# Kernel optimization log

Hardware: AMD Instinct MI355X
Metric: run time of the kernel (lower is better)

The kernel has to match this reference:

```python
import jax, jax.numpy as jnp
import numpy as np

PS = 8          # patch size
D_STATE = 16
D_CONV = 4
DT_RANK = 6     # ceil(96/16)
N_HEADS = 2
NEG = jnp.float32(-1e30)
_DIRS = np.array([[-1, 0], [1, 0], [0, -1], [0, 1]], np.int32)


def _ln(x, w, b, eps=1e-5):
    mu = x.mean(-1, keepdims=True)
    var = ((x - mu) ** 2).mean(-1, keepdims=True)
    return (x - mu) * jax.lax.rsqrt(var + eps) * w + b


def _vit_score_map(x, pos_embed, proj_w, proj_b, in_w, in_b, out_w, out_b,
                   ln1_w, ln1_b, ff1_w, ff1_b, ff2_w, ff2_b, ln2_w, ln2_b,
                   score_w, score_b):
    B, C, H, W = x.shape
    Hp, Wp = H // PS, W // PS
    N = Hp * Wp
    E = proj_w.shape[0]
    # F.unfold ordering: per patch the vector is (C, kr, kc) flattened
    patches = x.reshape(B, C, Hp, PS, Wp, PS).transpose(0, 2, 4, 1, 3, 5).reshape(B, N, C * PS * PS)
    patches = patches @ proj_w.T + proj_b
    if pos_embed.shape[1] != N:
        o = int(pos_embed.shape[1] ** 0.5)
        pe = jax.image.resize(pos_embed.reshape(1, o, o, E), (1, Hp, Wp, E), 'bilinear').reshape(1, N, E)
    else:
        pe = pos_embed
    patches = patches + 0.1 * pe
    # nn.TransformerEncoderLayer defaults: post-norm, ReLU, eval (no dropout)
    qkv = patches @ in_w.T + in_b
    q, k, v = jnp.split(qkv, 3, axis=-1)
    dh = E // N_HEADS
    def heads(t):
        return t.reshape(B, N, N_HEADS, dh).transpose(0, 2, 1, 3)
    q, k, v = heads(q), heads(k), heads(v)
    attn = jax.nn.softmax(jnp.einsum('bhqd,bhkd->bhqk', q, k) / np.float32(np.sqrt(dh)), axis=-1)
    ctx = jnp.einsum('bhqk,bhkd->bhqd', attn, v).transpose(0, 2, 1, 3).reshape(B, N, E)
    src = _ln(patches + (ctx @ out_w.T + out_b), ln1_w, ln1_b)
    ff = jax.nn.relu(src @ ff1_w.T + ff1_b) @ ff2_w.T + ff2_b
    src = _ln(src + ff, ln2_w, ln2_b)
    scores = jax.nn.sigmoid((src @ score_w.T + score_b)[..., 0])
    pvar = patches.var(axis=-1, ddof=1)          # torch.var is unbiased
    final = 0.7 * scores + 0.3 * jax.nn.sigmoid(pvar * 10.0)
    return final.reshape(B, Hp, Wp)


def _traversal(score):
    """Greedy adaptive patch traversal: start at global argmax, walk to the best
    unvisited 4-neighbor; on dead-end jump to the global argmax over unvisited."""
    Hp, Wp = score.shape
    n = Hp * Wp
    s = score.reshape(-1)
    dirs = jnp.asarray(_DIRS)
    start = jnp.argmax(s).astype(jnp.int32)
    visited0 = jnp.zeros((n,), bool).at[start].set(True)

    def step(carry, _):
        visited, cur = carry
        ci, cj = cur // Wp, cur % Wp
        ni, nj = ci + dirs[:, 0], cj + dirs[:, 1]
        valid = (ni >= 0) & (ni < Hp) & (nj >= 0) & (nj < Wp)
        nidx = (jnp.clip(ni, 0, Hp - 1) * Wp + jnp.clip(nj, 0, Wp - 1)).astype(jnp.int32)
        nsc = jnp.where(valid & ~visited[nidx], s[nidx], NEG)
        b = jnp.argmax(nsc)                       # first-max tie-break == '>' loop order
        jump = jnp.argmax(jnp.where(visited, NEG, s)).astype(jnp.int32)
        nxt = jnp.where(nsc[b] > NEG * 0.5, nidx[b], jump).astype(jnp.int32)
        return (visited.at[nxt].set(True), nxt), nxt

    _, rest = jax.lax.scan(step, (visited0, start), None, length=n - 1)
    return jnp.concatenate([start[None], rest])


def _mamba(u, in_w, conv_w, conv_b, xproj_w, dt_w, dt_b, A_log, D_skip, out_w):
    B, L, _ = u.shape
    d_in = conv_w.shape[0]
    xz = u @ in_w.T                               # (B,L,2*d_in)
    xx, z = jnp.split(xz, 2, axis=-1)
    # causal depthwise conv over sequence
    xc = jnp.pad(xx.transpose(0, 2, 1), ((0, 0), (0, 0), (D_CONV - 1, 0)))
    xc = jax.lax.conv_general_dilated(xc, conv_w, (1,), 'VALID',
                                      feature_group_count=d_in,
                                      dimension_numbers=('NCH', 'OIH', 'NCH'))
    xx = jax.nn.silu((xc + conv_b[None, :, None]).transpose(0, 2, 1))   # (B,L,d_in)
    dbl = xx @ xproj_w.T
    dt, Bm, Cm = jnp.split(dbl, [DT_RANK, DT_RANK + D_STATE], axis=-1)
    dt = jax.nn.softplus(dt @ dt_w.T + dt_b)      # (B,L,d_in)
    A = -jnp.exp(A_log)                           # (d_in, d_state)

    def step(h, inp):
        dt_t, B_t, C_t, x_t = inp                 # (B,d_in),(B,ds),(B,ds),(B,d_in)
        h = jnp.exp(dt_t[..., None] * A) * h + (dt_t * x_t)[..., None] * B_t[:, None, :]
        return h, jnp.einsum('bds,bs->bd', h, C_t)

    h0 = jnp.zeros((B, d_in, D_STATE), u.dtype)
    xs = (dt.transpose(1, 0, 2), Bm.transpose(1, 0, 2), Cm.transpose(1, 0, 2), xx.transpose(1, 0, 2))
    _, ys = jax.lax.scan(step, h0, xs)
    y = ys.transpose(1, 0, 2) + xx * D_skip
    return (y * jax.nn.silu(z)) @ out_w.T


def setup_inputs() -> dict:
    key = jax.random.key(0)
    ks = jax.random.split(key, 20)
    B, C, H, W = 2, 96, 128, 128
    E, FF = 96, 2048
    d_in, dr, ds, dc = 192, 6, 16, 4
    f32 = jnp.float32
    def w(k, shape, s=0.02):
        return jax.random.normal(k, shape, f32) * s
    return dict(
        x=jax.random.normal(ks[0], (B, C, H, W), f32),
        pe=w(ks[1], (B, H * W, C), 0.02),
        pos_embed=w(ks[2], (1, 784, E)),
        vit_proj_w=w(ks[3], (E, C * PS * PS)),
        vit_proj_b=jnp.zeros((E,), f32),
        attn_in_w=w(ks[4], (3 * E, E)),
        attn_in_b=jnp.zeros((3 * E,), f32),
        attn_out_w=w(ks[5], (E, E)),
        attn_out_b=jnp.zeros((E,), f32),
        ln1_w=jnp.ones((E,), f32), ln1_b=jnp.zeros((E,), f32),
        ff1_w=w(ks[6], (FF, E)), ff1_b=jnp.zeros((FF,), f32),
        ff2_w=w(ks[7], (E, FF)), ff2_b=jnp.zeros((E,), f32),
        ln2_w=jnp.ones((E,), f32), ln2_b=jnp.zeros((E,), f32),
        score_w=w(ks[8], (1, E)), score_b=jnp.zeros((1,), f32),
        norm_w=jnp.ones((C,), f32), norm_b=jnp.zeros((C,), f32),
        in_proj_w=w(ks[9], (2 * d_in, C)),
        conv_w=w(ks[10], (d_in, 1, dc), 0.1),
        conv_b=jnp.zeros((d_in,), f32),
        x_proj_w=w(ks[11], (dr + 2 * ds, d_in)),
        dt_w=w(ks[12], (d_in, dr)),
        dt_b=jnp.full((d_in,), -4.6, f32),        # softplus(dt_b) ~ 0.01 (mamba dt init)
        A_log=jnp.log(jnp.tile(jnp.arange(1, ds + 1, dtype=f32), (d_in, 1))),
        D_skip=jnp.ones((d_in,), f32),
        out_proj_w=w(ks[13], (C, d_in)),
    )


def reference(x, pe, pos_embed, vit_proj_w, vit_proj_b, attn_in_w, attn_in_b,
              attn_out_w, attn_out_b, ln1_w, ln1_b, ff1_w, ff1_b, ff2_w, ff2_b,
              ln2_w, ln2_b, score_w, score_b, norm_w, norm_b, in_proj_w,
              conv_w, conv_b, x_proj_w, dt_w, dt_b, A_log, D_skip, out_proj_w):
    B, C, H, W = x.shape
    n = H * W
    # Dynamic_Adaptive_Scan with the code's DCNv3Function-is-None fallback:
    # x = input_last, permuted back to channels-first => identity on x.
    x_adapted = x
    score_map = _vit_score_map(x_adapted, pos_embed, vit_proj_w, vit_proj_b,
                               attn_in_w, attn_in_b, attn_out_w, attn_out_b,
                               ln1_w, ln1_b, ff1_w, ff1_b, ff2_w, ff2_b,
                               ln2_w, ln2_b, score_w, score_b)
    order = jax.vmap(_traversal)(jax.lax.stop_gradient(score_map))    # (B, Hp*Wp)
    Hp, Wp = score_map.shape[1], score_map.shape[2]
    pi, pj = order // Wp, order % Wp
    # expand each patch into its PSxPS pixels in raster order
    offs = (jnp.arange(PS, dtype=jnp.int32)[:, None] * W + jnp.arange(PS, dtype=jnp.int32)[None, :]).reshape(-1)
    idx = ((pi * PS * W + pj * PS)[..., None] + offs).reshape(B, n)    # (B, n)
    x_tok = jnp.take_along_axis(x_adapted.reshape(B, C, n), idx[:, None, :], axis=2).transpose(0, 2, 1)
    pe_r = jnp.take_along_axis(pe, idx[..., None], axis=1)
    tokens = _ln(x_tok + pe_r, norm_w, norm_b)
    y = _mamba(tokens, in_proj_w, conv_w, conv_b, x_proj_w, dt_w, dt_b, A_log, D_skip, out_proj_w)
    # scatter back to spatial raster order
    out = jax.vmap(lambda yb, ib: jnp.zeros_like(yb).at[ib].set(yb))(y, idx)
    return out.transpose(0, 2, 1).reshape(B, C, H, W)
```

## Files before the change

kernel.cpp:

```cpp
#include <hip/hip_runtime.h>
#include <math.h>

#define BB 2
#define CC 96
#define HH 128
#define WW 128
#define PS 8
#define HP 16
#define WP 16
#define NPATCH 256
#define EE 96
#define FF 2048
#define DH 48
#define DIN 192
#define DR 6
#define DS 16
#define LL 16384
#define NCHUNK 512
#define CLEN 32
#define NSEG 16
#define SEGC 32
#define KTOT 6144
#define KSPLIT 32
#define KSL 192

__device__ __forceinline__ float sigmoid_acc(float x){ return 1.f/(1.f+expf(-x)); }
__device__ __forceinline__ float sigmoid_fast(float x){ return 1.f/(1.f+__expf(-x)); }

__global__ void k_resize_pe(const float* __restrict__ pos, float* __restrict__ pe16){
  int n = blockIdx.x;
  int oi = n / WP, oj = n % WP;
  int e = threadIdx.x;
  const float inv = 1.75f;
  float sfi = (oi + 0.5f)*inv - 0.5f;
  float sfj = (oj + 0.5f)*inv - 0.5f;
  int i0 = max(0, (int)ceilf(sfi - inv)), i1 = min(27, (int)floorf(sfi + inv));
  int j0 = max(0, (int)ceilf(sfj - inv)), j1 = min(27, (int)floorf(sfj + inv));
  float si = 0.f, sj = 0.f;
  for(int j=i0;j<=i1;j++) si += fmaxf(0.f, 1.f - fabsf(sfi - (float)j)/inv);
  for(int j=j0;j<=j1;j++) sj += fmaxf(0.f, 1.f - fabsf(sfj - (float)j)/inv);
  float acc = 0.f;
  for(int ji=i0;ji<=i1;ji++){
    float wv = fmaxf(0.f, 1.f - fabsf(sfi - (float)ji)/inv) / si;
    for(int jj=j0;jj<=j1;jj++){
      float wu = fmaxf(0.f, 1.f - fabsf(sfj - (float)jj)/inv);
      acc += wv * (wu/sj) * pos[(ji*28+jj)*EE + e];
    }
  }
  pe16[n*EE + e] = acc;
}

__global__ void k_wtr(const float* __restrict__ vw, float* __restrict__ Wt){
  __shared__ float t[64*97];
  int k0 = blockIdx.x*64;
  int tid = threadIdx.x;
  for(int i=tid;i<64*EE;i+=256){
    int e = i>>6, kk = i&63;
    t[kk*97 + e] = vw[(size_t)e*KTOT + k0 + kk];
  }
  __syncthreads();
  for(int i=tid;i<64*EE;i+=256){
    int kk = i/EE, e = i%EE;
    Wt[(size_t)(k0+kk)*EE + e] = t[kk*97 + e];
  }
}

__global__ __launch_bounds__(384) void k_pproj(const float* __restrict__ x,
    const float* __restrict__ Wt, float* __restrict__ part){
  __shared__ float As[16*196];
  int bidx = blockIdx.x;
  int ks = bidx & (KSPLIT-1);
  int pb = bidx >> 5;
  int b = pb >> 4, pi = pb & 15;
  int c0 = ks*3;
  int tid = threadIdx.x;
  for(int i=tid;i<24*128;i+=384){
    int row = i>>7;
    int col = i&127;
    int cl = row>>3, dr = row&7;
    float v = x[(((size_t)(b*CC + c0+cl))<<14) + (size_t)((pi*PS+dr)<<7) + col];
    As[(col>>3)*196 + cl*64 + dr*8 + (col&7)] = v;
  }
  __syncthreads();
  int e = tid % EE;
  int pq = tid / EE;
  const float* wp = Wt + (size_t)(ks*KSL)*EE + e;
  float acc0=0.f, acc1=0.f, acc2=0.f, acc3=0.f;
  const float4* A0 = (const float4*)(As + (pq*4+0)*196);
  const float4* A1 = (const float4*)(As + (pq*4+1)*196);
  const float4* A2 = (const float4*)(As + (pq*4+2)*196);
  const float4* A3 = (const float4*)(As + (pq*4+3)*196);
  #pragma unroll 4
  for(int k4=0;k4<48;k4++){
    float w0 = wp[(k4*4+0)*EE];
    float w1 = wp[(k4*4+1)*EE];
    float w2 = wp[(k4*4+2)*EE];
    float w3 = wp[(k4*4+3)*EE];
    float4 a;
    a = A0[k4]; acc0 += a.x*w0 + a.y*w1 + a.z*w2 + a.w*w3;
    a = A1[k4]; acc1 += a.x*w0 + a.y*w1 + a.z*w2 + a.w*w3;
    a = A2[k4]; acc2 += a.x*w0 + a.y*w1 + a.z*w2 + a.w*w3;
    a = A3[k4]; acc3 += a.x*w0 + a.y*w1 + a.z*w2 + a.w*w3;
  }
  size_t gp0 = (size_t)b*NPATCH + pi*WP + pq*4;
  part[((size_t)ks*512 + gp0+0)*EE + e] = acc0;
  part[((size_t)ks*512 + gp0+1)*EE + e] = acc1;
  part[((size_t)ks*512 + gp0+2)*EE + e] = acc2;
  part[((size_t)ks*512 + gp0+3)*EE + e] = acc3;
}

__global__ __launch_bounds__(320) void k_preduce_qkv(const float* __restrict__ part,
    const float* __restrict__ pb, const float* __restrict__ pe16,
    const float* __restrict__ inw, const float* __restrict__ inb,
    float* __restrict__ patches, float* __restrict__ pvar, float* __restrict__ qkv){
  int gp = blockIdx.x;
  int n = gp % NPATCH;
  int tid = threadIdx.x;
  __shared__ float a[EE];
  __shared__ float ps[2], pq2[2];
  float v = 0.f;
  if(tid < EE){
    float s = 0.f;
    #pragma unroll 8
    for(int ks=0;ks<KSPLIT;ks++) s += part[((size_t)ks*512 + gp)*EE + tid];
    v = s + pb[tid] + 0.1f*pe16[n*EE + tid];
    a[tid] = v;
    patches[(size_t)gp*EE + tid] = v;
  }
  if(tid < 128){
    float sv = v, sq = v*v;
    for(int off=32; off>0; off>>=1){ sv += __shfl_xor(sv, off); sq += __shfl_xor(sq, off); }
    if((tid&63)==0){ ps[tid>>6]=sv; pq2[tid>>6]=sq; }
  }
  __syncthreads();
  if(tid==0){
    float s = ps[0]+ps[1], qq = pq2[0]+pq2[1];
    float mu = s/EE;
    pvar[gp] = (qq - EE*mu*mu)/(EE-1);
  }
  if(tid < 288){
    const float4* ar = (const float4*)a;
    const float4* wr = (const float4*)(inw + (size_t)tid*EE);
    float4 s4 = {0.f,0.f,0.f,0.f};
    #pragma unroll
    for(int k=0;k<24;k++){
      float4 av=ar[k], wv=wr[k];
      s4.x += av.x*wv.x; s4.y += av.y*wv.y; s4.z += av.z*wv.z; s4.w += av.w*wv.w;
    }
    qkv[(size_t)gp*288 + tid] = inb[tid] + (s4.x+s4.y)+(s4.z+s4.w);
  }
}

__global__ void k_attn(const float* __restrict__ qkv, float* __restrict__ ctx){
  int gb = blockIdx.x;
  int i = gb % NPATCH; int h = (gb/NPATCH)&1; int b = gb/(NPATCH*2);
  int tid = threadIdx.x;
  __shared__ float q[DH];
  __shared__ float p[NPATCH];
  __shared__ float red[NPATCH];
  __shared__ float red2[4][DH];
  const float* base = qkv + (size_t)b*NPATCH*288;
  if(tid < DH) q[tid] = base[(size_t)i*288 + h*DH + tid];
  __syncthreads();
  float sc;
  {
    const float4* krow = (const float4*)(base + (size_t)tid*288 + 96 + h*DH);
    const float4* q4 = (const float4*)q;
    float4 s4 = {0.f,0.f,0.f,0.f};
    #pragma unroll
    for(int k=0;k<12;k++){
      float4 kv=krow[k], qv=q4[k];
      s4.x += qv.x*kv.x; s4.y += qv.y*kv.y; s4.z += qv.z*kv.z; s4.w += qv.w*kv.w;
    }
    sc = ((s4.x+s4.y)+(s4.z+s4.w)) * 0.14433756729740643f;
  }
  red[tid] = sc; __syncthreads();
  for(int st=128; st>0; st>>=1){ if(tid<st) red[tid]=fmaxf(red[tid],red[tid+st]); __syncthreads(); }
  float mx = red[0]; __syncthreads();
  float ev = expf(sc - mx);
  red[tid] = ev; __syncthreads();
  for(int st=128; st>0; st>>=1){ if(tid<st) red[tid]+=red[tid+st]; __syncthreads(); }
  float denom = red[0]; __syncthreads();
  p[tid] = ev/denom;
  __syncthreads();
  if(tid < 192){
    int jg = tid/DH, dd = tid%DH;
    const float* vb = base + 192 + h*DH + dd;
    float acc0 = 0.f, acc1 = 0.f;
    #pragma unroll 4
    for(int j=jg*64; j<jg*64+64; j+=2){
      acc0 += p[j]*vb[(size_t)j*288];
      acc1 += p[j+1]*vb[(size_t)(j+1)*288];
    }
    red2[jg][dd] = acc0+acc1;
  }
  __syncthreads();
  if(tid < DH){
    ctx[((size_t)b*NPATCH + i)*EE + h*DH + tid] =
      red2[0][tid]+red2[1][tid]+red2[2][tid]+red2[3][tid];
  }
}

__global__ void k_ln1(const float* __restrict__ ctx, const float* __restrict__ ow,
                      const float* __restrict__ ob, const float* __restrict__ patches,
                      const float* __restrict__ lw, const float* __restrict__ lb,
                      float* __restrict__ src1){
  int row = blockIdx.x; int tid = threadIdx.x;
  __shared__ float a[EE];
  __shared__ float ps[2], pq2[2], st[2];
  if(tid < EE) a[tid] = ctx[(size_t)row*EE + tid];
  __syncthreads();
  float o = 0.f;
  if(tid < EE){
    const float4* ar = (const float4*)a;
    const float4* wr = (const float4*)(ow + (size_t)tid*EE);
    float4 s4 = {0.f,0.f,0.f,0.f};
    #pragma unroll
    for(int k=0;k<24;k++){
      float4 av=ar[k], wv=wr[k];
      s4.x += av.x*wv.x; s4.y += av.y*wv.y; s4.z += av.z*wv.z; s4.w += av.w*wv.w;
    }
    o = ob[tid] + (s4.x+s4.y)+(s4.z+s4.w) + patches[(size_t)row*EE + tid];
  }
  float sv = o, sq = o*o;
  for(int off=32; off>0; off>>=1){ sv += __shfl_xor(sv, off); sq += __shfl_xor(sq, off); }
  if((tid&63)==0){ ps[tid>>6]=sv; pq2[tid>>6]=sq; }
  __syncthreads();
  if(tid==0){
    float s = ps[0]+ps[1], qq = pq2[0]+pq2[1];
    float mu = s/EE;
    st[0]=mu; st[1]=rsqrtf(qq/EE - mu*mu + 1e-5f);
  }
  __syncthreads();
  if(tid < EE) src1[(size_t)row*EE + tid] = (o-st[0])*st[1]*lw[tid] + lb[tid];
}

__global__ __launch_bounds__(512) void k_ff1(const float* __restrict__ src1,
    const float* __restrict__ w1, const float* __restrict__ b1, float* __restrict__ ffh){
  int row0 = blockIdx.x*2; int tid = threadIdx.x;
  const float4* a0 = (const float4*)(src1 + (size_t)row0*EE);
  const float4* a1 = (const float4*)(src1 + (size_t)(row0+1)*EE);
  for(int fo=0;fo<4;fo++){
    int f = fo*512 + tid;
    const float4* wr = (const float4*)(w1 + (size_t)f*EE);
    float bc = b1[f];
    float acc0=bc, acc1=bc;
    #pragma unroll
    for(int k=0;k<24;k++){
      float4 wv = wr[k];
      float4 av;
      av = a0[k]; acc0 += av.x*wv.x+av.y*wv.y+av.z*wv.z+av.w*wv.w;
      av = a1[k]; acc1 += av.x*wv.x+av.y*wv.y+av.z*wv.z+av.w*wv.w;
    }
    ffh[(size_t)(row0+0)*FF + f] = fmaxf(acc0, 0.f);
    ffh[(size_t)(row0+1)*FF + f] = fmaxf(acc1, 0.f);
  }
}

__global__ __launch_bounds__(384) void k_ff2(const float* __restrict__ ffh,
    const float* __restrict__ w2, const float* __restrict__ b2,
    const float* __restrict__ src1, float* __restrict__ src2){
  __shared__ float partl[8][EE];
  int row0 = blockIdx.x*2; int tid = threadIdx.x;
  int e = tid % EE, fg = tid / EE;
  const float4* wr = (const float4*)(w2 + (size_t)e*FF + fg*512);
  const float4* h0 = (const float4*)(ffh + (size_t)row0*FF + fg*512);
  const float4* h1 = (const float4*)(ffh + (size_t)(row0+1)*FF + fg*512);
  float acc0=0.f, acc1=0.f;
  #pragma unroll 4
  for(int k=0;k<128;k++){
    float4 wv = wr[k];
    float4 hv;
    hv = h0[k]; acc0 += hv.x*wv.x+hv.y*wv.y+hv.z*wv.z+hv.w*wv.w;
    hv = h1[k]; acc1 += hv.x*wv.x+hv.y*wv.y+hv.z*wv.z+hv.w*wv.w;
  }
  partl[0*4+fg][e] = acc0;
  partl[1*4+fg][e] = acc1;
  __syncthreads();
  if(tid < 192){
    int r = tid / EE, e2 = tid % EE;
    float s = partl[r*4+0][e2] + partl[r*4+1][e2] + partl[r*4+2][e2] + partl[r*4+3][e2];
    src2[(size_t)(row0+r)*EE + e2] = s + b2[e2] + src1[(size_t)(row0+r)*EE + e2];
  }
}

__global__ void k_ln2_score(const float* __restrict__ src2,
    const float* __restrict__ lw, const float* __restrict__ lb,
    const float* __restrict__ sw, const float* __restrict__ sb,
    const float* __restrict__ pvar, float* __restrict__ fscore){
  int row = blockIdx.x; int tid = threadIdx.x;
  float v = (tid < EE) ? src2[(size_t)row*EE + tid] : 0.f;
  float sv = v, sq = v*v;
  for(int off=32; off>0; off>>=1){ sv += __shfl_xor(sv, off); sq += __shfl_xor(sq, off); }
  __shared__ float ps[2], pq2[2], st[2];
  int wid = tid>>6;
  if((tid&63)==0){ ps[wid]=sv; pq2[wid]=sq; }
  __syncthreads();
  if(tid==0){
    float s = ps[0]+ps[1], qq = pq2[0]+pq2[1];
    float mu = s/EE;
    st[0]=mu; st[1]=rsqrtf(qq/EE - mu*mu + 1e-5f);
  }
  __syncthreads();
  float o = (tid < EE) ? ((v-st[0])*st[1]*lw[tid] + lb[tid]) * sw[tid] : 0.f;
  for(int off=32; off>0; off>>=1) o += __shfl_xor(o, off);
  if((tid&63)==0) ps[wid] = o;
  __syncthreads();
  if(tid==0){
    float acc = ps[0]+ps[1] + sb[0];
    fscore[row] = 0.7f*sigmoid_acc(acc) + 0.3f*sigmoid_acc(pvar[row]*10.f);
  }
}

__global__ void k_traversal(const float* __restrict__ fscore, int* __restrict__ order){
  int b = blockIdx.x; int lane = threadIdx.x;
  __shared__ float fsl[NPATCH];
  __shared__ int   sidxl[NPATCH];
  for(int k=lane;k<NPATCH;k+=64) fsl[k] = fscore[b*NPATCH+k];
  __syncthreads();
  {
    float s0=fsl[lane], s1=fsl[64+lane], s2=fsl[128+lane], s3=fsl[192+lane];
    int i0=lane, i1=64+lane, i2=128+lane, i3=192+lane;
    int c0=0,c1=0,c2=0,c3=0;
    for(int j=0;j<NPATCH;j++){
      float sj=fsl[j];
      c0 += (sj>s0 || (sj==s0 && j<i0)) ? 1:0;
      c1 += (sj>s1 || (sj==s1 && j<i1)) ? 1:0;
      c2 += (sj>s2 || (sj==s2 && j<i2)) ? 1:0;
      c3 += (sj>s3 || (sj==s3 && j<i3)) ? 1:0;
    }
    sidxl[c0]=i0; sidxl[c1]=i1; sidxl[c2]=i2; sidxl[c3]=i3;
  }
  __syncthreads();
  if(lane==0){
    int cur = sidxl[0];
    order[b*NPATCH] = cur;
    fsl[cur] = -1e30f;
    int ptr = 1;
    int jcand = sidxl[1];
    for(int step=1; step<NPATCH; step++){
      int ci = cur>>4, cj = cur&15;
      int a0 = (ci>0)  ? cur-16 : cur;
      int a1 = (ci<15) ? cur+16 : cur;
      int a2 = (cj>0)  ? cur-1  : cur;
      int a3 = (cj<15) ? cur+1  : cur;
      float n0 = fsl[a0];
      float n1 = fsl[a1];
      float n2 = fsl[a2];
      float n3 = fsl[a3];
      float bv = n0; int bi = a0;
      if(n1 > bv){ bv=n1; bi=a1; }
      if(n2 > bv){ bv=n2; bi=a2; }
      if(n3 > bv){ bv=n3; bi=a3; }
      int nxt = (bv > -1e29f) ? bi : jcand;
      fsl[nxt] = -1e30f;
      order[b*NPATCH + step] = nxt;
      cur = nxt;
      if(nxt == jcand && step < NPATCH-1){
        float jv;
        do { ptr++; jcand = sidxl[ptr]; jv = fsl[jcand]; } while(jv <= -1e29f);
      }
    }
  }
}

__global__ __launch_bounds__(256) void k_gather_ln(const float* __restrict__ x,
    const float* __restrict__ pe, const int* __restrict__ order,
    const float* __restrict__ nw, const float* __restrict__ nb,
    float* __restrict__ tokens){
  __shared__ float val[64*97];
  int gb = blockIdx.x; int b = gb >> 8; int r = gb & 255;
  int tid = threadIdx.x;
  int p = order[b*NPATCH + r]; int pi = p>>4, pj = p&15;
  for(int i=tid;i<96*64;i+=256){
    int c = i>>6, q = i&63;
    int dr = q>>3, dc = q&7;
    val[q*97 + c] = x[(((size_t)(b*CC + c))<<14) + (size_t)((pi*PS+dr)<<7) + pj*PS + dc];
  }
  __syncthreads();
  for(int i=tid;i<64*EE;i+=256){
    int q = i/EE, c = i%EE;
    int pix = ((pi*PS + (q>>3))<<7) + pj*PS + (q&7);
    val[q*97 + c] += pe[((size_t)b*(HH*WW) + pix)*CC + c];
  }
  __syncthreads();
  int wid = tid>>6, lane = tid&63;
  for(int t=wid; t<64; t+=4){
    float v1 = val[t*97 + lane];
    float v2 = (lane<32) ? val[t*97 + 64 + lane] : 0.f;
    float sv = v1+v2, sq = v1*v1 + v2*v2;
    for(int off=32; off>0; off>>=1){ sv += __shfl_xor(sv, off); sq += __shfl_xor(sq, off); }
    float mu = sv/EE;
    float rs = rsqrtf(sq/EE - mu*mu + 1e-5f);
    size_t tb = ((size_t)b*LL + r*64 + t)*EE;
    tokens[tb + lane] = (v1-mu)*rs*nw[lane] + nb[lane];
    if(lane < 32) tokens[tb + 64 + lane] = (v2-mu)*rs*nw[64+lane] + nb[64+lane];
  }
}

__global__ __launch_bounds__(768, 5) void k_inproj_conv(const float* __restrict__ tokens,
    const float* __restrict__ w, const float* __restrict__ cw, const float* __restrict__ cb,
    float* __restrict__ z, float* __restrict__ xc){
  __shared__ float a[35*EE];
  __shared__ float ps[12*384];
  __shared__ float xxl[35*DIN];
  int rb = blockIdx.x; size_t row0 = (size_t)rb*32;
  int l0 = (int)(row0 % LL);
  int tid = threadIdx.x;
  int kh = tid / 384;
  int col = tid - kh*384;
  {
    const float4* src = (const float4*)(tokens + (row0-3)*EE);
    float4* adst = (float4*)a;
    for(int idx=tid; idx<840; idx+=768){
      float4 v;
      if(l0==0 && idx<72){ v.x=0.f; v.y=0.f; v.z=0.f; v.w=0.f; }
      else v = src[idx];
      adst[idx] = v;
    }
  }
  float4 wv[12];
  const float4* wr4 = (const float4*)(w + (size_t)col*EE + kh*48);
  #pragma unroll
  for(int i=0;i<12;i++) wv[i] = wr4[i];
  __syncthreads();
  #pragma unroll
  for(int g=0; g<3; g++){
    float acc[12];
    #pragma unroll
    for(int r=0;r<12;r++){
      int gi = g*12 + r;
      if(gi < 35){
        const float4* ar = (const float4*)(a + gi*EE + kh*48);
        float4 s4 = {0.f,0.f,0.f,0.f};
        #pragma unroll
        for(int i=0;i<12;i++){
          float4 av = ar[i];
          s4.x += av.x*wv[i].x; s4.y += av.y*wv[i].y; s4.z += av.z*wv[i].z; s4.w += av.w*wv[i].w;
        }
        acc[r] = (s4.x+s4.y)+(s4.z+s4.w);
      } else acc[r] = 0.f;
    }
    if(kh==1){
      #pragma unroll
      for(int r=0;r<12;r++) if(g*12+r < 35) ps[r*384 + col] = acc[r];
    }
    __syncthreads();
    if(kh==0){
      #pragma unroll
      for(int r=0;r<12;r++){
        int gi = g*12 + r;
        if(gi < 35){
          float tot = acc[r] + ps[r*384 + col];
          if(col < DIN) xxl[gi*DIN + col] = tot;
          else if(gi >= 3) z[(row0 + gi - 3)*DIN + (col - DIN)] = tot;
        }
      }
    }
    __syncthreads();
  }
  #pragma unroll
  for(int it=0; it<8; it++){
    int idx = tid + it*768;
    int rr = idx / DIN, d = idx - rr*DIN;
    float v = cb[d]
      + cw[d*4+0]*xxl[(rr+0)*DIN + d]
      + cw[d*4+1]*xxl[(rr+1)*DIN + d]
      + cw[d*4+2]*xxl[(rr+2)*DIN + d]
      + cw[d*4+3]*xxl[(rr+3)*DIN + d];
    xc[(row0 + rr)*DIN + d] = v * sigmoid_fast(v);
  }
}

__global__ __launch_bounds__(320) void k_xproj(const float* __restrict__ xc, const float* __restrict__ xpw,
    const float* __restrict__ dtw, const float* __restrict__ dtb,
    float* __restrict__ dt, float* __restrict__ Bm, float* __restrict__ Cm){
  __shared__ float a[8][196];
  __shared__ float dbl[8][40];
  int rb = blockIdx.x; size_t row0 = (size_t)rb*8;
  int tid = threadIdx.x;
  for(int i=tid;i<8*DIN;i+=320){ int r=i/DIN, k=i%DIN; a[r][k] = xc[(row0+r)*DIN + k]; }
  __syncthreads();
  {
    int r = tid & 7, o = tid >> 3;
    if(o < 38){
      const float4* wr = (const float4*)(xpw + (size_t)o*DIN);
      const float4* ar = (const float4*)(a[r]);
      float4 s4 = {0.f,0.f,0.f,0.f};
      #pragma unroll
      for(int k=0;k<48;k++){
        float4 av=ar[k], wv=wr[k];
        s4.x += av.x*wv.x; s4.y += av.y*wv.y; s4.z += av.z*wv.z; s4.w += av.w*wv.w;
      }
      dbl[r][o] = (s4.x+s4.y)+(s4.z+s4.w);
    }
  }
  __syncthreads();
  for(int t=tid;t<8*DIN;t+=320){
    int r = t/DIN, d = t%DIN;
    float acc = dtb[d];
    #pragma unroll
    for(int j=0;j<DR;j++) acc += dbl[r][j]*dtw[d*DR+j];
    dt[(row0+r)*DIN + d] = fmaxf(acc, 0.f) + log1pf(__expf(-fabsf(acc)));
  }
  if(tid < 8*DS){
    int r = tid/DS, s = tid%DS;
    Bm[(row0+r)*DS + s] = dbl[r][6+s];
    Cm[(row0+r)*DS + s] = dbl[r][22+s];
  }
}

__global__ __launch_bounds__(192) void k_scan1(const float* __restrict__ dt,
    const float* __restrict__ xc, const float* __restrict__ Bm,
    const float* __restrict__ Alog, float* __restrict__ hend, float* __restrict__ sumdt){
  int blk = blockIdx.x;
  int b = blk >> 9, c = blk & (NCHUNK-1);
  int d = threadIdx.x;
  float A[16];
  {
    const float4* a4 = (const float4*)(Alog + d*DS);
    #pragma unroll
    for(int i=0;i<4;i++){
      float4 v = a4[i];
      A[i*4+0]=-expf(v.x); A[i*4+1]=-expf(v.y); A[i*4+2]=-expf(v.z); A[i*4+3]=-expf(v.w);
    }
  }
  float h[16];
  #pragma unroll
  for(int s=0;s<16;s++) h[s]=0.f;
  float sd = 0.f;
  size_t base = (size_t)b*LL + (size_t)c*CLEN;
  const float* dp = dt + base*DIN + d;
  const float* xp = xc + base*DIN + d;
  const float4* bp = (const float4*)(Bm + base*DS);
  for(int t=0;t<CLEN;t++){
    float dtv = dp[(size_t)t*DIN];
    float xv  = xp[(size_t)t*DIN];
    float4 b0=bp[t*4+0], b1=bp[t*4+1], b2=bp[t*4+2], b3=bp[t*4+3];
    float e[16];
    #pragma unroll
    for(int s=0;s<16;s++) e[s] = __expf(dtv*A[s]);
    float Bv[16] = {b0.x,b0.y,b0.z,b0.w,b1.x,b1.y,b1.z,b1.w,b2.x,b2.y,b2.z,b2.w,b3.x,b3.y,b3.z,b3.w};
    float dx = dtv*xv; sd += dtv;
    #pragma unroll
    for(int s=0;s<16;s++) h[s] = e[s]*h[s] + dx*Bv[s];
  }
  size_t o = ((size_t)c*BB + b)*DIN + d;
  float4* hp = (float4*)(hend + o*DS);
  hp[0] = make_float4(h[0],h[1],h[2],h[3]);
  hp[1] = make_float4(h[4],h[5],h[6],h[7]);
  hp[2] = make_float4(h[8],h[9],h[10],h[11]);
  hp[3] = make_float4(h[12],h[13],h[14],h[15]);
  sumdt[o] = sd;
}

__global__ __launch_bounds__(256) void k_scan2a(const float* __restrict__ hend,
    const float* __restrict__ sumdt, const float* __restrict__ Alog,
    float* __restrict__ segP, float* __restrict__ segH){
  int g = blockIdx.x*256 + threadIdx.x;
  int seg = g / 6144; int r = g % 6144;
  int b = r / 3072; int d = (r % 3072) >> 4; int s = r & 15;
  float A = -expf(Alog[d*DS + s]);
  float P = 1.f, H = 0.f;
  int c0 = seg*SEGC;
  for(int cc=0; cc<SEGC; cc+=4){
    float sd[4], he[4];
    #pragma unroll
    for(int j=0;j<4;j++){
      size_t o = ((size_t)(c0+cc+j)*BB + b)*DIN + d;
      sd[j] = sumdt[o]; he[j] = hend[o*DS + s];
    }
    #pragma unroll
    for(int j=0;j<4;j++){
      float aa = __expf(A*sd[j]);
      H = aa*H + he[j]; P *= aa;
    }
  }
  segP[seg*6144 + r] = P; segH[seg*6144 + r] = H;
}

__global__ void k_scan2b(const float* __restrict__ segP, const float* __restrict__ segH,
                         float* __restrict__ segHin){
  int r = blockIdx.x*256 + threadIdx.x;
  float P[NSEG], H[NSEG];
  #pragma unroll
  for(int sg=0; sg<NSEG; sg++){ P[sg]=segP[sg*6144+r]; H[sg]=segH[sg*6144+r]; }
  float h = 0.f;
  #pragma unroll
  for(int sg=0; sg<NSEG; sg++){
    segHin[sg*6144 + r] = h;
    h = P[sg]*h + H[sg];
  }
}

__global__ __launch_bounds__(256) void k_scan2c(float* __restrict__ hend,
    const float* __restrict__ sumdt, const float* __restrict__ Alog,
    const float* __restrict__ segHin){
  int g = blockIdx.x*256 + threadIdx.x;
  int seg = g / 6144; int r = g % 6144;
  int b = r / 3072; int d = (r % 3072) >> 4; int s = r & 15;
  float A = -expf(Alog[d*DS + s]);
  float h = segHin[seg*6144 + r];
  int c0 = seg*SEGC;
  for(int cc=0; cc<SEGC; cc+=4){
    float sd[4], he[4]; size_t oo[4];
    #pragma unroll
    for(int j=0;j<4;j++){
      oo[j] = ((size_t)(c0+cc+j)*BB + b)*DIN + d;
      sd[j] = sumdt[oo[j]]; he[j] = hend[oo[j]*DS + s];
    }
    #pragma unroll
    for(int j=0;j<4;j++){
      hend[oo[j]*DS + s] = h;
      float aa = __expf(A*sd[j]);
      h = aa*h + he[j];
    }
  }
}

__global__ __launch_bounds__(192) void k_scan3(const float* __restrict__ dt,
    const float* __restrict__ xc, const float* __restrict__ Bm, const float* __restrict__ Cm,
    const float* __restrict__ Alog, const float* __restrict__ hin,
    const float* __restrict__ Dskip, float* __restrict__ zg){
  int blk = blockIdx.x;
  int b = blk >> 9, c = blk & (NCHUNK-1);
  int d = threadIdx.x;
  float A[16];
  {
    const float4* a4 = (const float4*)(Alog + d*DS);
    #pragma unroll
    for(int i=0;i<4;i++){
      float4 v = a4[i];
      A[i*4+0]=-expf(v.x); A[i*4+1]=-expf(v.y); A[i*4+2]=-expf(v.z); A[i*4+3]=-expf(v.w);
    }
  }
  size_t o = ((size_t)c*BB + b)*DIN + d;
  float h[16];
  {
    const float4* hi = (const float4*)(hin + o*DS);
    #pragma unroll
    for(int i=0;i<4;i++){
      float4 v = hi[i];
      h[i*4+0]=v.x; h[i*4+1]=v.y; h[i*4+2]=v.z; h[i*4+3]=v.w;
    }
  }
  float Dv = Dskip[d];
  size_t base = (size_t)b*LL + (size_t)c*CLEN;
  const float* dp = dt + base*DIN + d;
  const float* xp = xc + base*DIN + d;
  float* zp = zg + base*DIN + d;
  const float4* bp = (const float4*)(Bm + base*DS);
  const float4* cp = (const float4*)(Cm + base*DS);
  for(int t=0;t<CLEN;t++){
    float dtv = dp[(size_t)t*DIN];
    float xv  = xp[(size_t)t*DIN];
    float zv  = zp[(size_t)t*DIN];
    float4 b0=bp[t*4+0], b1=bp[t*4+1], b2=bp[t*4+2], b3=bp[t*4+3];
    float4 c0=cp[t*4+0], c1=cp[t*4+1], c2=cp[t*4+2], c3=cp[t*4+3];
    float e[16];
    #pragma unroll
    for(int s=0;s<16;s++) e[s] = __expf(dtv*A[s]);
    float Bv[16] = {b0.x,b0.y,b0.z,b0.w,b1.x,b1.y,b1.z,b1.w,b2.x,b2.y,b2.z,b2.w,b3.x,b3.y,b3.z,b3.w};
    float Cv[16] = {c0.x,c0.y,c0.z,c0.w,c1.x,c1.y,c1.z,c1.w,c2.x,c2.y,c2.z,c2.w,c3.x,c3.y,c3.z,c3.w};
    float dx = dtv*xv;
    float y = 0.f;
    #pragma unroll
    for(int s=0;s<16;s++){ h[s] = e[s]*h[s] + dx*Bv[s]; y += h[s]*Cv[s]; }
    float yy = y + xv*Dv;
    zp[(size_t)t*DIN] = yy * (zv * sigmoid_fast(zv));
  }
}

__global__ __launch_bounds__(384) void k_outproj(const float* __restrict__ g,
    const float* __restrict__ w, float* __restrict__ ytok){
  __shared__ float a[16*DIN];
  __shared__ float psA[16*EE];
  __shared__ float psB[16*EE];
  int rb = blockIdx.x; size_t row0 = (size_t)rb*16;
  int tid = threadIdx.x;
  int col = tid % EE, kq = tid / EE;
  {
    const float4* src = (const float4*)(g + row0*DIN);
    float4* ad = (float4*)a;
    ad[tid] = src[tid];
    ad[tid+384] = src[tid+384];
  }
  float4 wv[12];
  const float4* wr4 = (const float4*)(w + (size_t)col*DIN + kq*48);
  #pragma unroll
  for(int i=0;i<12;i++) wv[i] = wr4[i];
  __syncthreads();
  float acc[16];
  for(int r=0;r<16;r++){
    const float4* ar = (const float4*)(a + r*DIN + kq*48);
    float4 s4 = {0.f,0.f,0.f,0.f};
    #pragma unroll
    for(int i=0;i<12;i++){
      float4 av = ar[i];
      s4.x += av.x*wv[i].x; s4.y += av.y*wv[i].y; s4.z += av.z*wv[i].z; s4.w += av.w*wv[i].w;
    }
    acc[r] = (s4.x+s4.y)+(s4.z+s4.w);
  }
  if(kq==1){
    for(int r=0;r<16;r++) psA[r*EE+col] = acc[r];
  }
  if(kq==3){
    for(int r=0;r<16;r++) psB[r*EE+col] = acc[r];
  }
  __syncthreads();
  if(kq==0){
    for(int r=0;r<16;r++) acc[r] += psA[r*EE+col];
  }
  if(kq==2){
    for(int r=0;r<16;r++) acc[r] += psB[r*EE+col];
  }
  __syncthreads();
  if(kq==2){
    for(int r=0;r<16;r++) psA[r*EE+col] = acc[r];
  }
  __syncthreads();
  if(kq==0){
    for(int r=0;r<16;r++) ytok[(row0+r)*EE + col] = acc[r] + psA[r*EE+col];
  }
}

__global__ __launch_bounds__(256) void k_scatter(const float* __restrict__ ytok,
    const int* __restrict__ order, float* __restrict__ out){
  __shared__ float yt[64*100];
  int gb = blockIdx.x; int b = gb>>8, r = gb&255;
  int p = order[b*NPATCH + r]; int pi = p>>4, pj = p&15;
  int tid = threadIdx.x;
  for(int i=tid;i<64*24;i+=256){
    int q = i/24, c4 = i%24;
    float4 v = ((const float4*)(ytok + ((size_t)b*LL + r*64 + q)*EE))[c4];
    ((float4*)(yt + q*100))[c4] = v;
  }
  __syncthreads();
  int q = tid&63; int cg = tid>>6;
  int pix = ((pi*PS + (q>>3))<<7) + pj*PS + (q&7);
  for(int c=cg;c<CC;c+=4){
    out[(((size_t)(b*CC + c))<<14) + pix] = yt[q*100 + c];
  }
}

extern "C" void kernel_launch(void* const* d_in, const int* in_sizes, int n_in,
                              void* d_out, int out_size, void* d_ws, size_t ws_size,
                              hipStream_t stream){
  (void)in_sizes; (void)n_in; (void)out_size; (void)ws_size;
  const float* x    = (const float*)d_in[0];
  const float* pe   = (const float*)d_in[1];
  const float* pos  = (const float*)d_in[2];
  const float* vw   = (const float*)d_in[3];
  const float* vb   = (const float*)d_in[4];
  const float* inw  = (const float*)d_in[5];
  const float* inb  = (const float*)d_in[6];
  const float* ow   = (const float*)d_in[7];
  const float* ob   = (const float*)d_in[8];
  const float* l1w  = (const float*)d_in[9];
  const float* l1b  = (const float*)d_in[10];
  const float* f1w  = (const float*)d_in[11];
  const float* f1b  = (const float*)d_in[12];
  const float* f2w  = (const float*)d_in[13];
  const float* f2b  = (const float*)d_in[14];
  const float* l2w  = (const float*)d_in[15];
  const float* l2b  = (const float*)d_in[16];
  const float* sw   = (const float*)d_in[17];
  const float* sb   = (const float*)d_in[18];
  const float* nw   = (const float*)d_in[19];
  const float* nb   = (const float*)d_in[20];
  const float* ipw  = (const float*)d_in[21];
  const float* cw   = (const float*)d_in[22];
  const float* cb   = (const float*)d_in[23];
  const float* xpw  = (const float*)d_in[24];
  const float* dtw  = (const float*)d_in[25];
  const float* dtbp = (const float*)d_in[26];
  const float* alog = (const float*)d_in[27];
  const float* dsk  = (const float*)d_in[28];
  const float* opw  = (const float*)d_in[29];
  float* out = (float*)d_out;

  char* wsb = (char*)d_ws;
  size_t off = 0;
  auto alloc = [&](size_t nfloats)->void*{
    void* p = (void*)(wsb + off);
    off += ((nfloats*sizeof(float) + 255) & ~(size_t)255);
    return p;
  };
  float* pe16    = (float*)alloc(256*96);
  float* patches = (float*)alloc(512*96);
  float* pvar    = (float*)alloc(512);
  float* qkv     = (float*)alloc((size_t)512*288);
  float* ctxb    = (float*)alloc(512*96);
  float* src1    = (float*)alloc(512*96);
  float* ffh     = (float*)alloc((size_t)512*2048);
  float* fscore  = (float*)alloc(512);
  int*   order   = (int*)  alloc(512);
  float* tokens  = (float*)alloc((size_t)2*16384*96);
  float* xxb     = (float*)alloc((size_t)2*16384*192);
  float* zb      = (float*)alloc((size_t)2*16384*192);
  float* xcb     = (float*)alloc((size_t)2*16384*192);
  float* Bmat    = (float*)alloc((size_t)2*16384*16);
  float* Cmat    = (float*)alloc((size_t)2*16384*16);
  float* sumdt   = (float*)alloc((size_t)NCHUNK*2*192);
  float* segP    = (float*)alloc((size_t)NSEG*6144);
  float* segH    = (float*)alloc((size_t)NSEG*6144);
  float* segHin  = (float*)alloc((size_t)NSEG*6144);
  float* dtbuf = xxb;
  float* Wt    = xxb;
  float* part  = tokens;
  float* hend  = tokens;
  float* hin   = hend;
  float* ytok  = tokens;
  float* src2  = qkv;

  k_resize_pe   <<<256,   96, 0, stream>>>(pos, pe16);
  k_wtr         <<<96,   256, 0, stream>>>(vw, Wt);
  k_pproj       <<<1024, 384, 0, stream>>>(x, Wt, part);
  k_preduce_qkv <<<512,  320, 0, stream>>>(part, vb, pe16, inw, inb, patches, pvar, qkv);
  k_attn        <<<1024, 256, 0, stream>>>(qkv, ctxb);
  k_ln1         <<<512,  128, 0, stream>>>(ctxb, ow, ob, patches, l1w, l1b, src1);
  k_ff1         <<<256,  512, 0, stream>>>(src1, f1w, f1b, ffh);
  k_ff2         <<<256,  384, 0, stream>>>(ffh, f2w, f2b, src1, src2);
  k_ln2_score   <<<512,  128, 0, stream>>>(src2, l2w, l2b, sw, sb, pvar, fscore);
  k_traversal   <<<2,     64, 0, stream>>>(fscore, order);
  k_gather_ln   <<<512,  256, 0, stream>>>(x, pe, order, nw, nb, tokens);
  k_inproj_conv <<<1024, 768, 0, stream>>>(tokens, ipw, cw, cb, zb, xcb);
  k_xproj       <<<4096, 320, 0, stream>>>(xcb, xpw, dtw, dtbp, dtbuf, Bmat, Cmat);
  k_scan1       <<<1024, 192, 0, stream>>>(dtbuf, xcb, Bmat, alog, hend, sumdt);
  k_scan2a      <<<384,  256, 0, stream>>>(hend, sumdt, alog, segP, segH);
  k_scan2b      <<<24,   256, 0, stream>>>(segP, segH, segHin);
  k_scan2c      <<<384,  256, 0, stream>>>(hend, sumdt, alog, segHin);
  k_scan3       <<<1024, 192, 0, stream>>>(dtbuf, xcb, Bmat, Cmat, alog, hin, dsk, zb);
  k_outproj     <<<2048, 384, 0, stream>>>(zb, opw, ytok);
  k_scatter     <<<512,  256, 0, stream>>>(ytok, order, out);
}
```

Baseline: 506.4 us.

## Fuse attention with out-proj+LN1, fuse FF2 with LN2+score, buffer traversal order

Merges the per-head attention kernel with the output projection and first LayerNorm, so each block now handles both heads for one query row and keeps the context vector in shared memory. It also folds the second LayerNorm and score head into the FF2 kernel, and has the traversal write its order to shared memory before a single coalesced copy out. This removes two kernel launches and the round trips through the ctx and src2 buffers. In exchange, the attention grid is halved, so there is less parallelism and a longer serial V-accumulation per thread.

After: 504.3 us. No clear change (-0.4%).

```diff
diff --git a/kernel.cpp b/kernel.cpp
--- a/kernel.cpp
+++ b/kernel.cpp
@@ -151,68 +151,73 @@
   }
 }
 
-__global__ void k_attn(const float* __restrict__ qkv, float* __restrict__ ctx){
+__global__ __launch_bounds__(256) void k_attn_ln1(const float* __restrict__ qkv,
+    const float* __restrict__ ow, const float* __restrict__ ob,
+    const float* __restrict__ patches, const float* __restrict__ lw,
+    const float* __restrict__ lb, float* __restrict__ src1){
   int gb = blockIdx.x;
-  int i = gb % NPATCH; int h = (gb/NPATCH)&1; int b = gb/(NPATCH*2);
+  int i = gb & 255, b = gb >> 8;
   int tid = threadIdx.x;
-  __shared__ float q[DH];
-  __shared__ float p[NPATCH];
-  __shared__ float red[NPATCH];
-  __shared__ float red2[4][DH];
+  __shared__ float q[EE];
+  __shared__ float2 red[NPATCH];
+  __shared__ float p0[NPATCH], p1[NPATCH];
+  __shared__ float part[2][EE];
+  __shared__ float ctxs[EE];
+  __shared__ float ps[2], pq2[2], st[2];
   const float* base = qkv + (size_t)b*NPATCH*288;
-  if(tid < DH) q[tid] = base[(size_t)i*288 + h*DH + tid];
-  __syncthreads();
-  float sc;
+  if(tid < EE) q[tid] = base[(size_t)i*288 + tid];
+  __syncthreads();
+  float sc0, sc1;
   {
-    const float4* krow = (const float4*)(base + (size_t)tid*288 + 96 + h*DH);
+    const float4* krow = (const float4*)(base + (size_t)tid*288 + 96);
     const float4* q4 = (const float4*)q;
-    float4 s4 = {0.f,0.f,0.f,0.f};
+    float4 a0 = {0.f,0.f,0.f,0.f}, a1 = {0.f,0.f,0.f,0.f};
     #pragma unroll
     for(int k=0;k<12;k++){
       float4 kv=krow[k], qv=q4[k];
-      s4.x += qv.x*kv.x; s4.y += qv.y*kv.y; s4.z += qv.z*kv.z; s4.w += qv.w*kv.w;
-    }
-    sc = ((s4.x+s4.y)+(s4.z+s4.w)) * 0.14433756729740643f;
-  }
-  red[tid] = sc; __syncthreads();
-  for(int st=128; st>0; st>>=1){ if(tid<st) red[tid]=fmaxf(red[tid],red[tid+st]); __syncthreads(); }
-  float mx = red[0]; __syncthreads();
-  float ev = expf(sc - mx);
-  red[tid] = ev; __syncthreads();
-  for(int st=128; st>0; st>>=1){ if(tid<st) red[tid]+=red[tid+st]; __syncthreads(); }
-  float denom = red[0]; __syncthreads();
-  p[tid] = ev/denom;
+      a0.x += qv.x*kv.x; a0.y += qv.y*kv.y; a0.z += qv.z*kv.z; a0.w += qv.w*kv.w;
+    }
+    #pragma unroll
+    for(int k=12;k<24;k++){
+      float4 kv=krow[k], qv=q4[k];
+      a1.x += qv.x*kv.x; a1.y += qv.y*kv.y; a1.z += qv.z*kv.z; a1.w += qv.w*kv.w;
+    }
+    sc0 = ((a0.x+a0.y)+(a0.z+a0.w)) * 0.14433756729740643f;
+    sc1 = ((a1.x+a1.y)+(a1.z+a1.w)) * 0.14433756729740643f;
+  }
+  red[tid] = make_float2(sc0, sc1); __syncthreads();
+  for(int stp=128; stp>0; stp>>=1){
+    if(tid<stp){ float2 o=red[tid+stp]; red[tid].x=fmaxf(red[tid].x,o.x); red[tid].y=fmaxf(red[tid].y,o.y); }
+    __syncthreads();
+  }
+  float2 mx = red[0]; __syncthreads();
+  float ev0 = expf(sc0 - mx.x), ev1 = expf(sc1 - mx.y);
+  red[tid] = make_float2(ev0, ev1); __syncthreads();
+  for(int stp=128; stp>0; stp>>=1){
+    if(tid<stp){ float2 o=red[tid+stp]; red[tid].x+=o.x; red[tid].y+=o.y; }
+    __syncthreads();
+  }
+  float2 dn = red[0]; __syncthreads();
+  p0[tid] = ev0/dn.x; p1[tid] = ev1/dn.y;
   __syncthreads();
   if(tid < 192){
-    int jg = tid/DH, dd = tid%DH;
-    const float* vb = base + 192 + h*DH + dd;
+    int dd = tid % EE, jh = tid / EE;
+    const float* vb = base + 192 + dd;
+    const float* pp = (dd < DH) ? p0 : p1;
     float acc0 = 0.f, acc1 = 0.f;
     #pragma unroll 4
-    for(int j=jg*64; j<jg*64+64; j+=2){
-      acc0 += p[j]*vb[(size_t)j*288];
-      acc1 += p[j+1]*vb[(size_t)(j+1)*288];
-    }
-    red2[jg][dd] = acc0+acc1;
-  }
-  __syncthreads();
-  if(tid < DH){
-    ctx[((size_t)b*NPATCH + i)*EE + h*DH + tid] =
-      red2[0][tid]+red2[1][tid]+red2[2][tid]+red2[3][tid];
-  }
-}
-
-__global__ void k_ln1(const float* __restrict__ ctx, const float* __restrict__ ow,
-                      const float* __restrict__ ob, const float* __restrict__ patches,
-                      const float* __restrict__ lw, const float* __restrict__ lb,
-                      float* __restrict__ src1){
-  int row = blockIdx.x; int tid = threadIdx.x;
-  __shared__ float a[EE];
-  __shared__ float ps[2], pq2[2], st[2];
-  if(tid < EE) a[tid] = ctx[(size_t)row*EE + tid];
+    for(int j=jh*128; j<jh*128+128; j+=2){
+      acc0 += pp[j]*vb[(size_t)j*288];
+      acc1 += pp[j+1]*vb[(size_t)(j+1)*288];
+    }
+    part[jh][dd] = acc0+acc1;
+  }
+  __syncthreads();
+  if(tid < EE) ctxs[tid] = part[0][tid] + part[1][tid];
   __syncthreads();
   float o = 0.f;
   if(tid < EE){
-    const float4* ar = (const float4*)a;
+    const float4* ar = (const float4*)ctxs;
     const float4* wr = (const float4*)(ow + (size_t)tid*EE);
     float4 s4 = {0.f,0.f,0.f,0.f};
     #pragma unroll
@@ -220,11 +225,13 @@
       float4 av=ar[k], wv=wr[k];
       s4.x += av.x*wv.x; s4.y += av.y*wv.y; s4.z += av.z*wv.z; s4.w += av.w*wv.w;
     }
-    o = ob[tid] + (s4.x+s4.y)+(s4.z+s4.w) + patches[(size_t)row*EE + tid];
-  }
-  float sv = o, sq = o*o;
-  for(int off=32; off>0; off>>=1){ sv += __shfl_xor(sv, off); sq += __shfl_xor(sq, off); }
-  if((tid&63)==0){ ps[tid>>6]=sv; pq2[tid>>6]=sq; }
+    o = ob[tid] + (s4.x+s4.y)+(s4.z+s4.w) + patches[(size_t)gb*EE + tid];
+  }
+  if(tid < 128){
+    float sv = o, sq = o*o;
+    for(int off=32; off>0; off>>=1){ sv += __shfl_xor(sv, off); sq += __shfl_xor(sq, off); }
+    if((tid&63)==0){ ps[tid>>6]=sv; pq2[tid>>6]=sq; }
+  }
   __syncthreads();
   if(tid==0){
     float s = ps[0]+ps[1], qq = pq2[0]+pq2[1];
@@ -232,7 +239,7 @@
     st[0]=mu; st[1]=rsqrtf(qq/EE - mu*mu + 1e-5f);
   }
   __syncthreads();
-  if(tid < EE) src1[(size_t)row*EE + tid] = (o-st[0])*st[1]*lw[tid] + lb[tid];
+  if(tid < EE) src1[(size_t)gb*EE + tid] = (o-st[0])*st[1]*lw[tid] + lb[tid];
 }
 
 __global__ __launch_bounds__(512) void k_ff1(const float* __restrict__ src1,
@@ -257,10 +264,15 @@
   }
 }
 
-__global__ __launch_bounds__(384) void k_ff2(const float* __restrict__ ffh,
+__global__ __launch_bounds__(384) void k_ff2_score(const float* __restrict__ ffh,
     const float* __restrict__ w2, const float* __restrict__ b2,
-    const float* __restrict__ src1, float* __restrict__ src2){
+    const float* __restrict__ src1, const float* __restrict__ lw,
+    const float* __restrict__ lb, const float* __restrict__ sw,
+    const float* __restrict__ sb, const float* __restrict__ pvar,
+    float* __restrict__ fscore){
   __shared__ float partl[8][EE];
+  __shared__ float s2[2][EE];
+  __shared__ float psr[2][2], pqr[2][2], str[2][2];
   int row0 = blockIdx.x*2; int tid = threadIdx.x;
   int e = tid % EE, fg = tid / EE;
   const float4* wr = (const float4*)(w2 + (size_t)e*FF + fg*512);
@@ -280,35 +292,33 @@
   if(tid < 192){
     int r = tid / EE, e2 = tid % EE;
     float s = partl[r*4+0][e2] + partl[r*4+1][e2] + partl[r*4+2][e2] + partl[r*4+3][e2];
-    src2[(size_t)(row0+r)*EE + e2] = s + b2[e2] + src1[(size_t)(row0+r)*EE + e2];
-  }
-}
-
-__global__ void k_ln2_score(const float* __restrict__ src2,
-    const float* __restrict__ lw, const float* __restrict__ lb,
-    const float* __restrict__ sw, const float* __restrict__ sb,
-    const float* __restrict__ pvar, float* __restrict__ fscore){
-  int row = blockIdx.x; int tid = threadIdx.x;
-  float v = (tid < EE) ? src2[(size_t)row*EE + tid] : 0.f;
-  float sv = v, sq = v*v;
-  for(int off=32; off>0; off>>=1){ sv += __shfl_xor(sv, off); sq += __shfl_xor(sq, off); }
-  __shared__ float ps[2], pq2[2], st[2];
-  int wid = tid>>6;
-  if((tid&63)==0){ ps[wid]=sv; pq2[wid]=sq; }
-  __syncthreads();
-  if(tid==0){
-    float s = ps[0]+ps[1], qq = pq2[0]+pq2[1];
+    s2[r][e2] = s + b2[e2] + src1[(size_t)(row0+r)*EE + e2];
+  }
+  __syncthreads();
+  int g = tid >> 7, t = tid & 127;
+  float v = 0.f;
+  if(g < 2){
+    v = (t < EE) ? s2[g][t] : 0.f;
+    float sv = v, sq = v*v;
+    for(int off=32; off>0; off>>=1){ sv += __shfl_xor(sv, off); sq += __shfl_xor(sq, off); }
+    if((t&63)==0){ psr[g][t>>6]=sv; pqr[g][t>>6]=sq; }
+  }
+  __syncthreads();
+  if(g < 2 && t == 0){
+    float s = psr[g][0]+psr[g][1], qq = pqr[g][0]+pqr[g][1];
     float mu = s/EE;
-    st[0]=mu; st[1]=rsqrtf(qq/EE - mu*mu + 1e-5f);
-  }
-  __syncthreads();
-  float o = (tid < EE) ? ((v-st[0])*st[1]*lw[tid] + lb[tid]) * sw[tid] : 0.f;
-  for(int off=32; off>0; off>>=1) o += __shfl_xor(o, off);
-  if((tid&63)==0) ps[wid] = o;
-  __syncthreads();
-  if(tid==0){
-    float acc = ps[0]+ps[1] + sb[0];
-    fscore[row] = 0.7f*sigmoid_acc(acc) + 0.3f*sigmoid_acc(pvar[row]*10.f);
+    str[g][0]=mu; str[g][1]=rsqrtf(qq/EE - mu*mu + 1e-5f);
+  }
+  __syncthreads();
+  if(g < 2){
+    float o = (t < EE) ? ((v-str[g][0])*str[g][1]*lw[t] + lb[t]) * sw[t] : 0.f;
+    for(int off=32; off>0; off>>=1) o += __shfl_xor(o, off);
+    if((t&63)==0) psr[g][t>>6] = o;
+  }
+  __syncthreads();
+  if(g < 2 && t == 0){
+    float acc = psr[g][0]+psr[g][1] + sb[0];
+    fscore[row0+g] = 0.7f*sigmoid_acc(acc) + 0.3f*sigmoid_acc(pvar[row0+g]*10.f);
   }
 }
 
@@ -316,6 +326,7 @@
   int b = blockIdx.x; int lane = threadIdx.x;
   __shared__ float fsl[NPATCH];
   __shared__ int   sidxl[NPATCH];
+  __shared__ int   ordl[NPATCH];
   for(int k=lane;k<NPATCH;k+=64) fsl[k] = fscore[b*NPATCH+k];
   __syncthreads();
   {
@@ -334,7 +345,7 @@
   __syncthreads();
   if(lane==0){
     int cur = sidxl[0];
-    order[b*NPATCH] = cur;
+    ordl[0] = cur;
     fsl[cur] = -1e30f;
     int ptr = 1;
     int jcand = sidxl[1];
@@ -354,7 +365,7 @@
       if(n3 > bv){ bv=n3; bi=a3; }
       int nxt = (bv > -1e29f) ? bi : jcand;
       fsl[nxt] = -1e30f;
-      order[b*NPATCH + step] = nxt;
+      ordl[step] = nxt;
       cur = nxt;
       if(nxt == jcand && step < NPATCH-1){
         float jv;
@@ -362,6 +373,8 @@
       }
     }
   }
+  __syncthreads();
+  for(int k=lane;k<NPATCH;k+=64) order[b*NPATCH+k] = ordl[k];
 }
 
 __global__ __launch_bounds__(256) void k_gather_ln(const float* __restrict__ x,
@@ -790,7 +803,6 @@
   float* patches = (float*)alloc(512*96);
   float* pvar    = (float*)alloc(512);
   float* qkv     = (float*)alloc((size_t)512*288);
-  float* ctxb    = (float*)alloc(512*96);
   float* src1    = (float*)alloc(512*96);
   float* ffh     = (float*)alloc((size_t)512*2048);
   float* fscore  = (float*)alloc(512);
@@ -811,17 +823,14 @@
   float* hend  = tokens;
   float* hin   = hend;
   float* ytok  = tokens;
-  float* src2  = qkv;
 
   k_resize_pe   <<<256,   96, 0, stream>>>(pos, pe16);
   k_wtr         <<<96,   256, 0, stream>>>(vw, Wt);
   k_pproj       <<<1024, 384, 0, stream>>>(x, Wt, part);
   k_preduce_qkv <<<512,  320, 0, stream>>>(part, vb, pe16, inw, inb, patches, pvar, qkv);
-  k_attn        <<<1024, 256, 0, stream>>>(qkv, ctxb);
-  k_ln1         <<<512,  128, 0, stream>>>(ctxb, ow, ob, patches, l1w, l1b, src1);
+  k_attn_ln1    <<<512,  256, 0, stream>>>(qkv, ow, ob, patches, l1w, l1b, src1);
   k_ff1         <<<256,  512, 0, stream>>>(src1, f1w, f1b, ffh);
-  k_ff2         <<<256,  384, 0, stream>>>(ffh, f2w, f2b, src1, src2);
-  k_ln2_score   <<<512,  128, 0, stream>>>(src2, l2w, l2b, sw, sb, pvar, fscore);
+  k_ff2_score   <<<256,  384, 0, stream>>>(ffh, f2w, f2b, src1, l2w, l2b, sw, sb, pvar, fscore);
   k_traversal   <<<2,     64, 0, stream>>>(fscore, order);
   k_gather_ln   <<<512,  256, 0, stream>>>(x, pe, order, nw, nb, tokens);
   k_inproj_conv <<<1024, 768, 0, stream>>>(tokens, ipw, cw, cb, zb, xcb);
```
